# Optimization experiments

Measured on AMD Instinct MI355X. Metric: run time of the kernel, lower is better.

## Reference

```python
import jax, jax.numpy as jnp
import numpy as np

N_PART = 22
N_DIM = 3
H0 = 8
H_SIZE = H0 + 1  # + time condition
HID = 64
N_LAYERS = 4
B = 1024


def _base_edges(n):
    rows, cols = [], []
    for i in range(n):
        for j in range(i + 1, n):
            rows += [i, j]
            cols += [j, i]
    return np.asarray(rows, np.int32), np.asarray(cols, np.int32)


def _batched_edges(n_batch, n_nodes):
    r0, c0 = _base_edges(n_nodes)
    offs = (np.arange(n_batch, dtype=np.int32) * n_nodes)[:, None]
    rows = (r0[None, :] + offs).reshape(-1)
    cols = (c0[None, :] + offs).reshape(-1)
    return jnp.asarray(rows), jnp.asarray(cols)


def setup_inputs() -> dict:
    key = jax.random.key(0)
    ks = jax.random.split(key, 24)
    s = 0.1
    L = N_LAYERS
    d = {
        't': jax.random.uniform(ks[0], (B, 1), jnp.float32),
        'xs': jax.random.normal(ks[1], (B, N_PART * N_DIM), jnp.float32),
        'h_initial': jax.random.normal(ks[2], (N_PART, H0), jnp.float32),
        'emb_w': jax.random.normal(ks[3], (H_SIZE, HID), jnp.float32) * s,
        'emb_b': jnp.zeros((HID,), jnp.float32),
        'emb_out_w': jax.random.normal(ks[4], (HID, H_SIZE), jnp.float32) * s,
        'emb_out_b': jnp.zeros((H_SIZE,), jnp.float32),
        # edge_mlp: in = 2*HID + 1 (radial) + 1 (edge_attr) = 130
        'edge_w1': jax.random.normal(ks[5], (L, 2 * HID + 2, HID), jnp.float32) * s,
        'edge_b1': jnp.zeros((L, HID), jnp.float32),
        'edge_w2': jax.random.normal(ks[6], (L, HID, HID), jnp.float32) * s,
        'edge_b2': jnp.zeros((L, HID), jnp.float32),
        # node_mlp: in = HID (h) + HID (agg) = 128
        'node_w1': jax.random.normal(ks[7], (L, 2 * HID, HID), jnp.float32) * s,
        'node_b1': jnp.zeros((L, HID), jnp.float32),
        'node_w2': jax.random.normal(ks[8], (L, HID, HID), jnp.float32) * s,
        'node_b2': jnp.zeros((L, HID), jnp.float32),
        # coord_mlp: Lin(HID,HID) -> SiLU -> Lin(HID,1, no bias, xavier gain 0.001)
        'coord_w1': jax.random.normal(ks[9], (L, HID, HID), jnp.float32) * s,
        'coord_b1': jnp.zeros((L, HID), jnp.float32),
        'coord_w2': jax.random.normal(ks[10], (L, HID, 1), jnp.float32) * 0.001,
    }
    return d


def _egnn_forward(t, xs, h_initial, emb_w, emb_b, emb_out_w, emb_out_b,
                  edge_w1, edge_b1, edge_w2, edge_b2,
                  node_w1, node_b1, node_w2, node_b2,
                  coord_w1, coord_b1, coord_w2, rows, cols):
    silu = jax.nn.silu
    n_batch = xs.shape[0]
    N = n_batch * N_PART
    x0 = xs[:, :N_PART * N_DIM].reshape(N, N_DIM)

    # node features: atom features tiled over batch + time column
    h = jnp.tile(h_initial[None], (n_batch, 1, 1)).reshape(N, H0)
    t_nodes = jnp.repeat(t.reshape(n_batch, 1), N_PART, axis=0)  # (N,1)
    h = jnp.concatenate([h, t_nodes], axis=-1)  # (N, H_SIZE)

    # static edge attribute: squared distance at input coords
    d0 = x0[rows] - x0[cols]
    edge_attr = jnp.sum(d0 * d0, axis=-1, keepdims=True)  # (E,1)

    h = h @ emb_w + emb_b  # embedding
    x = x0
    for i in range(N_LAYERS):
        diff = x[rows] - x[cols]                       # (E,3)
        radial = jnp.sum(diff * diff, -1, keepdims=True)
        diff = diff / jnp.sqrt(radial + 1e-8)          # norm_diff=True
        ef = jnp.concatenate([h[rows], h[cols], radial, edge_attr], -1)
        m = silu(ef @ edge_w1[i] + edge_b1[i])
        m = silu(m @ edge_w2[i] + edge_b2[i])          # edge messages (E,HID)
        # equivariant coordinate update (tanh=False)
        scal = silu(m @ coord_w1[i] + coord_b1[i]) @ coord_w2[i]  # (E,1)
        x = x + jax.ops.segment_sum(diff * scal, rows, num_segments=N)
        # node update with residual (recurrent=True)
        agg = jax.ops.segment_sum(m, rows, num_segments=N)
        hn = silu(jnp.concatenate([h, agg], -1) @ node_w1[i] + node_b1[i])
        h = h + (hn @ node_w2[i] + node_b2[i])
    _ = h @ emb_out_w + emb_out_b  # embedding_out (h output unused by EGNN_AD2_CV)

    vel = (x - x0).reshape(n_batch, N_PART, N_DIM)
    vel = vel - jnp.mean(vel, axis=1, keepdims=True)   # remove_mean
    return vel.reshape(n_batch, N_PART * N_DIM)


def reference(t, xs, h_initial, emb_w, emb_b, emb_out_w, emb_out_b,
              edge_w1, edge_b1, edge_w2, edge_b2,
              node_w1, node_b1, node_w2, node_b2,
              coord_w1, coord_b1, coord_w2):
    rows, cols = _batched_edges(xs.shape[0], N_PART)
    return _egnn_forward(t, xs, h_initial, emb_w, emb_b, emb_out_w, emb_out_b,
                         edge_w1, edge_b1, edge_w2, edge_b2,
                         node_w1, node_b1, node_w2, node_b2,
                         coord_w1, coord_b1, coord_w2, rows, cols)
```

## Files before the change

kernel.cpp:

```cpp
#include <hip/hip_runtime.h>
#include <hip/hip_bf16.h>

#define NPART 22
#define NDEG  21
#define NEDGE 462
#define HID   64
#define NLAYERS 4
#define NSTRIPB 29
#define MW2S  72

typedef __attribute__((ext_vector_type(8))) short bf16x8;
typedef __attribute__((ext_vector_type(4))) float f32x4;
typedef __attribute__((ext_vector_type(4))) unsigned int u32x4;

__device__ __forceinline__ float silu_f(float v) {
    return __fdividef(v, 1.0f + __expf(-v));
}
__device__ __forceinline__ unsigned short bfu(float v) {
    return __bfloat16_as_ushort(__float2bfloat16(v));
}
__device__ __forceinline__ float bf2f(unsigned h) { return __uint_as_float(h << 16); }

__device__ __forceinline__ void split8(const float* va, bf16x8& hi, bf16x8& lo) {
    #pragma unroll
    for (int i = 0; i < 8; ++i) {
        unsigned short h = bfu(va[i]);
        hi[i] = (short)h;
        lo[i] = (short)bfu(va[i] - bf2f(h));
    }
}

__global__ void prep_wfrag(const float* __restrict__ edge_w2,
                           const float* __restrict__ coord_w1,
                           unsigned* __restrict__ wfrag)
{
    const int m = blockIdx.x;
    const int l = threadIdx.x;
    const int L = m >> 1;
    const float* W = (m & 1) ? (coord_w1 + L*HID*HID) : (edge_w2 + L*HID*HID);
    const int kg = l >> 4, j0 = l & 15;
    u32x4* ws4 = (u32x4*)wfrag;
    #pragma unroll
    for (int nt = 0; nt < 4; ++nt) {
        #pragma unroll
        for (int c = 0; c < 2; ++c) {
            u32x4 p;
            #pragma unroll
            for (int pi = 0; pi < 4; ++pi) {
                int k = c*32 + kg*8 + 2*pi;
                float v0 = W[k*HID + nt*16 + j0];
                float v1 = W[(k+1)*HID + nt*16 + j0];
                p[pi] = (unsigned)bfu(v0) | ((unsigned)bfu(v1) << 16);
            }
            ws4[m*512 + (nt*2 + c)*64 + l] = p;
        }
    }
}

__global__ void prep_nfrag(const float* __restrict__ node_w1,
                           const float* __restrict__ node_w2,
                           const float* __restrict__ edge_w1,
                           unsigned* __restrict__ nfrag)
{
    const int b = blockIdx.x;
    const int L = b >> 2, mat = b & 3;
    const int l = threadIdx.x;
    const int kg = l >> 4, j0 = l & 15;
    u32x4* nf = (u32x4*)nfrag + (size_t)L*80*64;
    const float* W; int nc, base;
    if      (mat == 0) { W = node_w1 + L*2*HID*HID;            nc = 4; base = 0;  }
    else if (mat == 1) { W = node_w2 + L*HID*HID;              nc = 2; base = 16; }
    else if (mat == 2) { W = edge_w1 + (L+1)*130*HID;          nc = 2; base = 24; }
    else               { W = edge_w1 + (L+1)*130*HID + 64*HID; nc = 2; base = 32; }
    for (int nt = 0; nt < 4; ++nt) {
        for (int c = 0; c < nc; ++c) {
            u32x4 ph, pl;
            #pragma unroll
            for (int pi = 0; pi < 4; ++pi) {
                int k = c*32 + kg*8 + 2*pi;
                float v0 = W[k*HID + nt*16 + j0];
                float v1 = W[(k+1)*HID + nt*16 + j0];
                unsigned h0 = bfu(v0), h1 = bfu(v1);
                unsigned l0 = bfu(v0 - bf2f(h0)), l1 = bfu(v1 - bf2f(h1));
                ph[pi] = h0 | (h1 << 16);
                pl[pi] = l0 | (l1 << 16);
            }
            int idx = base + nt*nc + c;
            nf[(size_t)idx*64 + l] = ph;
            nf[(size_t)(40 + idx)*64 + l] = pl;
        }
    }
}

__global__ __launch_bounds__(256, 4)
void k_init(const float* __restrict__ t_in, const float* __restrict__ xs,
            const float* __restrict__ h_init,
            const float* __restrict__ emb_w, const float* __restrict__ emb_b,
            const float* __restrict__ edge_w1, const float* __restrict__ edge_b1,
            float* __restrict__ xw, float* __restrict__ hw,
            float* __restrict__ Hrw, float* __restrict__ Hcw, int NT)
{
    __shared__ __align__(16) float hbuf[4][68];
    const int w = threadIdx.x >> 6, l = threadIdx.x & 63;
    const int n = blockIdx.x*4 + w;
    if (n >= NT) return;
    const int bidx = n / NPART, p = n - bidx*NPART;
    float hv = emb_b[l] + t_in[bidx]*emb_w[8*HID + l];
    #pragma unroll
    for (int k = 0; k < 8; ++k) hv += h_init[p*8 + k]*emb_w[k*HID + l];
    hw[(size_t)n*HID + l] = hv;
    hbuf[w][l] = hv;
    float accr = edge_b1[l], accc = 0.f;
    #pragma unroll 4
    for (int k = 0; k < HID; ++k) {
        float hk = hbuf[w][k];
        accr += hk*edge_w1[k*HID + l];
        accc += hk*edge_w1[(HID + k)*HID + l];
    }
    Hrw[(size_t)n*HID + l] = accr;
    Hcw[(size_t)n*HID + l] = accc;
    if (l < 3) xw[n*3 + l] = xs[n*3 + l];
}

__global__ __launch_bounds__(256, 4)
void k_edgeA(const float* __restrict__ edge_w1v,
             const float* __restrict__ edge_b2L,
             const float* __restrict__ coord_b1L,
             const float* __restrict__ coord_w2L,
             const unsigned* __restrict__ wfrag,
             const float* __restrict__ xs,
             const float* __restrict__ xw,
             const float* __restrict__ Hrw,
             const float* __restrict__ Hcw,
             float* __restrict__ aggpart,
             float* __restrict__ scalg,
             int nstrips, int Lmat)
{
    __shared__ __align__(16) float vecs[5][64];
    __shared__ __align__(16) unsigned short mwall[4][16*MW2S];
    __shared__ __align__(16) float xst[4][2][68];

    const int tid = threadIdx.x, l = tid & 63, w = tid >> 6;
    const int kg = l >> 4, j0 = l & 15;

    for (int i = tid; i < 320; i += 256) {
        int a = i >> 6, o = i & 63; float v;
        if      (a == 0) v = edge_w1v[o];
        else if (a == 1) v = edge_w1v[64 + o];
        else if (a == 2) v = edge_b2L[o];
        else if (a == 3) v = coord_b1L[o];
        else             v = coord_w2L[o];
        vecs[a][o] = v;
    }
    __syncthreads();

    const int sid = blockIdx.x*4 + w;
    if (sid >= nstrips) return;
    const int batch = sid / NSTRIPB, s = sid - batch*NSTRIPB;
    const int e0 = s*16;
    const int ecnt = (NEDGE - e0 < 16) ? (NEDGE - e0) : 16;
    const int n0 = e0 / NDEG;

    {
        const int base = batch*(NPART*3);
        xst[w][0][l] = xw[base + l];
        xst[w][1][l] = xs[base + l];
        if (l < 2) { xst[w][0][64+l] = xw[base+64+l]; xst[w][1][64+l] = xs[base+64+l]; }
    }

    int eg = e0 + j0; if (eg >= NEDGE) eg = NEDGE - 1;
    const int a  = eg / NDEG;
    const int r  = eg - a*NDEG;
    const int bb = r + (r >= a ? 1 : 0);
    float d0 = xst[w][0][a*3+0] - xst[w][0][bb*3+0];
    float d1 = xst[w][0][a*3+1] - xst[w][0][bb*3+1];
    float d2 = xst[w][0][a*3+2] - xst[w][0][bb*3+2];
    float rad = d0*d0 + d1*d1 + d2*d2;
    float g0 = xst[w][1][a*3+0] - xst[w][1][bb*3+0];
    float g1 = xst[w][1][a*3+1] - xst[w][1][bb*3+1];
    float g2 = xst[w][1][a*3+2] - xst[w][1][bb*3+2];
    float eav = g0*g0 + g1*g1 + g2*g2;

    const u32x4* ws4 = (const u32x4*)wfrag;
    const u32x4* wb1 = ws4 + (size_t)(Lmat*2    )*512 + l;
    const u32x4* wb2 = ws4 + (size_t)(Lmat*2 + 1)*512 + l;
    bf16x8 BW1[4][2];
    #pragma unroll
    for (int nt = 0; nt < 4; ++nt) {
        BW1[nt][0] = __builtin_bit_cast(bf16x8, wb1[(nt*2 + 0)*64]);
        BW1[nt][1] = __builtin_bit_cast(bf16x8, wb1[(nt*2 + 1)*64]);
    }

    bf16x8 Ah[2], Al[2];
    {
        const float* hrp = Hrw + (size_t)(batch*NPART + a)*HID;
        const float* hcp = Hcw + (size_t)(batch*NPART + bb)*HID;
        #pragma unroll
        for (int c = 0; c < 2; ++c) {
            const int k0 = c*32 + kg*8;
            float4 ra = *(const float4*)(hrp + k0);
            float4 rb = *(const float4*)(hrp + k0 + 4);
            float4 ca = *(const float4*)(hcp + k0);
            float4 cb = *(const float4*)(hcp + k0 + 4);
            float4 va = *(const float4*)&vecs[0][k0];
            float4 vb = *(const float4*)&vecs[0][k0 + 4];
            float4 ua = *(const float4*)&vecs[1][k0];
            float4 ub = *(const float4*)&vecs[1][k0 + 4];
            float tv[8];
            tv[0] = silu_f(ra.x + ca.x + rad*va.x + eav*ua.x);
            tv[1] = silu_f(ra.y + ca.y + rad*va.y + eav*ua.y);
            tv[2] = silu_f(ra.z + ca.z + rad*va.z + eav*ua.z);
            tv[3] = silu_f(ra.w + ca.w + rad*va.w + eav*ua.w);
            tv[4] = silu_f(rb.x + cb.x + rad*vb.x + eav*ub.x);
            tv[5] = silu_f(rb.y + cb.y + rad*vb.y + eav*ub.y);
            tv[6] = silu_f(rb.z + cb.z + rad*vb.z + eav*ub.z);
            tv[7] = silu_f(rb.w + cb.w + rad*vb.w + eav*ub.w);
            split8(tv, Ah[c], Al[c]);
        }
    }

    f32x4 acc[4];
    #pragma unroll
    for (int nt = 0; nt < 4; ++nt) {
        f32x4 z = {0.f, 0.f, 0.f, 0.f};
        z = __builtin_amdgcn_mfma_f32_16x16x32_bf16(Ah[0], BW1[nt][0], z, 0, 0, 0);
        z = __builtin_amdgcn_mfma_f32_16x16x32_bf16(Al[0], BW1[nt][0], z, 0, 0, 0);
        z = __builtin_amdgcn_mfma_f32_16x16x32_bf16(Ah[1], BW1[nt][1], z, 0, 0, 0);
        z = __builtin_amdgcn_mfma_f32_16x16x32_bf16(Al[1], BW1[nt][1], z, 0, 0, 0);
        acc[nt] = z;
    }

    bf16x8 B2[4][2];
    #pragma unroll
    for (int nt = 0; nt < 4; ++nt) {
        B2[nt][0] = __builtin_bit_cast(bf16x8, wb2[(nt*2 + 0)*64]);
        B2[nt][1] = __builtin_bit_cast(bf16x8, wb2[(nt*2 + 1)*64]);
    }

    int abn[4], emask[4];
    #pragma unroll
    for (int r2 = 0; r2 < 4; ++r2) {
        int e2 = kg*4 + r2;
        int eg2 = e0 + e2; if (eg2 >= NEDGE) eg2 = NEDGE - 1;
        abn[r2] = eg2 / NDEG;
        emask[r2] = (e2 < ecnt);
    }
    unsigned short* mw = mwall[w];
    float p0[4] = {0.f,0.f,0.f,0.f}, p1[4] = {0.f,0.f,0.f,0.f};
    #pragma unroll
    for (int nt = 0; nt < 4; ++nt) {
        int j = nt*16 + j0;
        float bv = vecs[2][j];
        #pragma unroll
        for (int r2 = 0; r2 < 4; ++r2) {
            float mv = silu_f(acc[nt][r2] + bv);
            mw[(kg*4 + r2)*MW2S + j] = bfu(mv);
            float msk = emask[r2] ? mv : 0.f;
            if (abn[r2] == n0)     p0[nt] += msk;
            if (abn[r2] == n0 + 1) p1[nt] += msk;
        }
    }
    #pragma unroll
    for (int nt = 0; nt < 4; ++nt) {
        p0[nt] += __shfl_xor(p0[nt], 16);
        p0[nt] += __shfl_xor(p0[nt], 32);
        p1[nt] += __shfl_xor(p1[nt], 16);
        p1[nt] += __shfl_xor(p1[nt], 32);
    }
    {
        float* apb = aggpart + (size_t)(batch*NSTRIPB + s)*128;
        if (kg == 0) {
            #pragma unroll
            for (int nt = 0; nt < 4; ++nt) apb[nt*16 + j0] = p0[nt];
        } else if (kg == 1) {
            #pragma unroll
            for (int nt = 0; nt < 4; ++nt) apb[64 + nt*16 + j0] = p1[nt];
        }
    }

    bf16x8 A2h[2];
    {
        const unsigned short* arp = mw + j0*MW2S;
        A2h[0] = *(const bf16x8*)(arp + kg*8);
        A2h[1] = *(const bf16x8*)(arp + 32 + kg*8);
    }

    f32x4 acc2[4];
    #pragma unroll
    for (int nt = 0; nt < 4; ++nt) {
        f32x4 z = {0.f, 0.f, 0.f, 0.f};
        z = __builtin_amdgcn_mfma_f32_16x16x32_bf16(A2h[0], B2[nt][0], z, 0, 0, 0);
        z = __builtin_amdgcn_mfma_f32_16x16x32_bf16(A2h[1], B2[nt][1], z, 0, 0, 0);
        acc2[nt] = z;
    }

    float pr[4] = {0.f,0.f,0.f,0.f};
    #pragma unroll
    for (int nt = 0; nt < 4; ++nt) {
        int j = nt*16 + j0;
        float cb = vecs[3][j], cw = vecs[4][j];
        #pragma unroll
        for (int r2 = 0; r2 < 4; ++r2)
            pr[r2] += silu_f(acc2[nt][r2] + cb) * cw;
    }
    #pragma unroll
    for (int off = 8; off > 0; off >>= 1) {
        #pragma unroll
        for (int r2 = 0; r2 < 4; ++r2)
            pr[r2] += __shfl_xor(pr[r2], off);
    }
    if (j0 == 0) {
        #pragma unroll
        for (int r2 = 0; r2 < 4; ++r2) {
            int e2 = kg*4 + r2;
            if (e2 < ecnt) scalg[(size_t)batch*464 + e0 + e2] = pr[r2];
        }
    }
}

__global__ __launch_bounds__(256, 4)
void k_dx(const float* __restrict__ scalg, float* __restrict__ xw, int NB)
{
    __shared__ float xstd[4][68], dxd[4][68];
    const int tid = threadIdx.x, l = tid & 63, w = tid >> 6;
    const int batch = blockIdx.x*4 + w;
    if (batch >= NB) return;
    xstd[w][l] = xw[batch*66 + ((l < 66) ? l : 0)];
    if (l < 2) xstd[w][64 + l] = xw[batch*66 + 64 + l];
    dxd[w][l] = 0.f;
    if (l < 4) dxd[w][64 + l] = 0.f;
    for (int e = l; e < NEDGE; e += 64) {
        int a = e / NDEG, r = e - a*NDEG;
        int bb = r + (r >= a ? 1 : 0);
        float d0 = xstd[w][a*3+0] - xstd[w][bb*3+0];
        float d1 = xstd[w][a*3+1] - xstd[w][bb*3+1];
        float d2 = xstd[w][a*3+2] - xstd[w][bb*3+2];
        float inv = rsqrtf(d0*d0 + d1*d1 + d2*d2 + 1e-8f);
        float sc = scalg[(size_t)batch*464 + e] * inv;
        atomicAdd(&dxd[w][a*3+0], d0*sc);
        atomicAdd(&dxd[w][a*3+1], d1*sc);
        atomicAdd(&dxd[w][a*3+2], d2*sc);
    }
    if (l < 64) xw[batch*66 + ((l < 66) ? l : 0)] = xstd[w][l] + dxd[w][l];
    if (l < 2)  xw[batch*66 + 64 + l] = xstd[w][64 + l] + dxd[w][64 + l];
}

__global__ __launch_bounds__(256, 2)
void k_nodeM(const unsigned* __restrict__ nfragL,
             const float* __restrict__ nb1p, const float* __restrict__ nb2p,
             const float* __restrict__ eb1p,
             const float* __restrict__ aggpart,
             float* __restrict__ hw,
             float* __restrict__ Hrw, float* __restrict__ Hcw,
             int NT, int nstripN)
{
    __shared__ __align__(16) float hT[4][16][68];
    __shared__ __align__(16) float hnT[4][16][68];
    const int tid = threadIdx.x, l = tid & 63, w = tid >> 6;
    const int kg = l >> 4, j0 = l & 15;
    const int sid = blockIdx.x*4 + w;
    if (sid >= nstripN) return;

    {
        int row = l >> 2, cc = (l & 3) << 4;
        int nd = sid*16 + row; if (nd >= NT) nd = NT - 1;
        const float* src = hw + (size_t)nd*HID + cc;
        *(float4*)&hT[w][row][cc]      = *(const float4*)(src);
        *(float4*)&hT[w][row][cc + 4]  = *(const float4*)(src + 4);
        *(float4*)&hT[w][row][cc + 8]  = *(const float4*)(src + 8);
        *(float4*)&hT[w][row][cc + 12] = *(const float4*)(src + 12);
    }

    const int ndl  = sid*16 + j0;
    const int ndc  = (ndl < NT) ? ndl : NT - 1;
    const int bidx = ndc / NPART, p = ndc - bidx*NPART;

    bf16x8 A1h[4], A1l[4];
    #pragma unroll
    for (int c = 0; c < 2; ++c) {
        float tv[8];
        #pragma unroll
        for (int i = 0; i < 8; ++i) tv[i] = hT[w][j0][c*32 + kg*8 + i];
        split8(tv, A1h[c], A1l[c]);
    }
    {
        const int smin = (NDEG*p) >> 4;
        const int smax = (NDEG*p + 20) >> 4;
        #pragma unroll
        for (int c = 2; c < 4; ++c) {
            const int k0a = (c - 2)*32 + kg*8;
            float tv[8] = {0.f,0.f,0.f,0.f,0.f,0.f,0.f,0.f};
            for (int s = smin; s <= smax; ++s) {
                int slot = (p == (s*16)/NDEG) ? 0 : 1;
                const float* ap = aggpart + (size_t)(bidx*NSTRIPB + s)*128 + slot*64 + k0a;
                float4 qa = *(const float4*)ap;
                float4 qb = *(const float4*)(ap + 4);
                tv[0] += qa.x; tv[1] += qa.y; tv[2] += qa.z; tv[3] += qa.w;
                tv[4] += qb.x; tv[5] += qb.y; tv[6] += qb.z; tv[7] += qb.w;
            }
            split8(tv, A1h[c], A1l[c]);
        }
    }

    const u32x4* nf = (const u32x4*)nfragL;
    #define NBF(idx) __builtin_bit_cast(bf16x8, nf[(size_t)(idx)*64 + l])

    f32x4 acc1[4];
    #pragma unroll
    for (int nt = 0; nt < 4; ++nt) {
        f32x4 z = {0.f, 0.f, 0.f, 0.f};
        #pragma unroll
        for (int c = 0; c < 4; ++c) {
            bf16x8 bh = NBF(nt*4 + c), bl = NBF(40 + nt*4 + c);
            z = __builtin_amdgcn_mfma_f32_16x16x32_bf16(A1h[c], bh, z, 0, 0, 0);
            z = __builtin_amdgcn_mfma_f32_16x16x32_bf16(A1l[c], bh, z, 0, 0, 0);
            z = __builtin_amdgcn_mfma_f32_16x16x32_bf16(A1h[c], bl, z, 0, 0, 0);
        }
        acc1[nt] = z;
    }
    #pragma unroll
    for (int nt = 0; nt < 4; ++nt) {
        float bv = nb1p[nt*16 + j0];
        #pragma unroll
        for (int r2 = 0; r2 < 4; ++r2)
            hnT[w][kg*4 + r2][nt*16 + j0] = silu_f(acc1[nt][r2] + bv);
    }

    bf16x8 A2h[2], A2l[2];
    #pragma unroll
    for (int c = 0; c < 2; ++c) {
        float tv[8];
        #pragma unroll
        for (int i = 0; i < 8; ++i) tv[i] = hnT[w][j0][c*32 + kg*8 + i];
        split8(tv, A2h[c], A2l[c]);
    }
    f32x4 acc2[4];
    #pragma unroll
    for (int nt = 0; nt < 4; ++nt) {
        f32x4 z = {0.f, 0.f, 0.f, 0.f};
        #pragma unroll
        for (int c = 0; c < 2; ++c) {
            bf16x8 bh = NBF(16 + nt*2 + c), bl = NBF(56 + nt*2 + c);
            z = __builtin_amdgcn_mfma_f32_16x16x32_bf16(A2h[c], bh, z, 0, 0, 0);
            z = __builtin_amdgcn_mfma_f32_16x16x32_bf16(A2l[c], bh, z, 0, 0, 0);
            z = __builtin_amdgcn_mfma_f32_16x16x32_bf16(A2h[c], bl, z, 0, 0, 0);
        }
        acc2[nt] = z;
    }
    #pragma unroll
    for (int nt = 0; nt < 4; ++nt) {
        float bv = nb2p[nt*16 + j0];
        #pragma unroll
        for (int r2 = 0; r2 < 4; ++r2) {
            int row = kg*4 + r2, col = nt*16 + j0;
            float hv = hT[w][row][col] + acc2[nt][r2] + bv;
            hnT[w][row][col] = hv;
            int nd = sid*16 + row;
            if (nd < NT) hw[(size_t)nd*HID + col] = hv;
        }
    }

    bf16x8 A3h[2], A3l[2];
    #pragma unroll
    for (int c = 0; c < 2; ++c) {
        float tv[8];
        #pragma unroll
        for (int i = 0; i < 8; ++i) tv[i] = hnT[w][j0][c*32 + kg*8 + i];
        split8(tv, A3h[c], A3l[c]);
    }
    f32x4 accR[4], accC[4];
    #pragma unroll
    for (int nt = 0; nt < 4; ++nt) {
        f32x4 zr = {0.f,0.f,0.f,0.f}, zc = {0.f,0.f,0.f,0.f};
        #pragma unroll
        for (int c = 0; c < 2; ++c) {
            bf16x8 brh = NBF(24 + nt*2 + c), brl = NBF(64 + nt*2 + c);
            bf16x8 bch = NBF(32 + nt*2 + c), bcl = NBF(72 + nt*2 + c);
            zr = __builtin_amdgcn_mfma_f32_16x16x32_bf16(A3h[c], brh, zr, 0, 0, 0);
            zr = __builtin_amdgcn_mfma_f32_16x16x32_bf16(A3l[c], brh, zr, 0, 0, 0);
            zr = __builtin_amdgcn_mfma_f32_16x16x32_bf16(A3h[c], brl, zr, 0, 0, 0);
            zc = __builtin_amdgcn_mfma_f32_16x16x32_bf16(A3h[c], bch, zc, 0, 0, 0);
            zc = __builtin_amdgcn_mfma_f32_16x16x32_bf16(A3l[c], bch, zc, 0, 0, 0);
            zc = __builtin_amdgcn_mfma_f32_16x16x32_bf16(A3h[c], bcl, zc, 0, 0, 0);
        }
        accR[nt] = zr; accC[nt] = zc;
    }
    #pragma unroll
    for (int nt = 0; nt < 4; ++nt) {
        float bv = eb1p[nt*16 + j0];
        #pragma unroll
        for (int r2 = 0; r2 < 4; ++r2) {
            int row = kg*4 + r2, col = nt*16 + j0;
            int nd = sid*16 + row;
            if (nd < NT) {
                Hrw[(size_t)nd*HID + col] = accR[nt][r2] + bv;
                Hcw[(size_t)nd*HID + col] = accC[nt][r2];
            }
        }
    }
    #undef NBF
}

__global__ void k_final(const float* __restrict__ xw, const float* __restrict__ xs,
                        const float* __restrict__ scalg, float* __restrict__ out)
{
    __shared__ float xstB[68], dxB[68], vb[68], mv3[3];
    const int b = blockIdx.x, t = threadIdx.x;
    if (t < 66) xstB[t] = xw[b*66 + t];
    if (t < 68) dxB[t] = 0.f;
    __syncthreads();
    for (int e = t; e < NEDGE; e += 256) {
        int a = e / NDEG, r = e - a*NDEG;
        int bb = r + (r >= a ? 1 : 0);
        float d0 = xstB[a*3+0] - xstB[bb*3+0];
        float d1 = xstB[a*3+1] - xstB[bb*3+1];
        float d2 = xstB[a*3+2] - xstB[bb*3+2];
        float inv = rsqrtf(d0*d0 + d1*d1 + d2*d2 + 1e-8f);
        float sc = scalg[(size_t)b*464 + e] * inv;
        atomicAdd(&dxB[a*3+0], d0*sc);
        atomicAdd(&dxB[a*3+1], d1*sc);
        atomicAdd(&dxB[a*3+2], d2*sc);
    }
    __syncthreads();
    if (t < 66) vb[t] = xstB[t] + dxB[t] - xs[b*66 + t];
    __syncthreads();
    if (t < 3) {
        float s = 0.f;
        #pragma unroll
        for (int p = 0; p < NPART; ++p) s += vb[p*3 + t];
        mv3[t] = s / (float)NPART;
    }
    __syncthreads();
    if (t < 66) out[b*66 + t] = vb[t] - mv3[t % 3];
}

extern "C" void kernel_launch(void* const* d_in, const int* in_sizes, int n_in,
                              void* d_out, int out_size, void* d_ws, size_t ws_size,
                              hipStream_t stream) {
    const float* t_in     = (const float*)d_in[0];
    const float* xs       = (const float*)d_in[1];
    const float* h_init   = (const float*)d_in[2];
    const float* emb_w    = (const float*)d_in[3];
    const float* emb_b    = (const float*)d_in[4];
    const float* edge_w1  = (const float*)d_in[7];
    const float* edge_b1  = (const float*)d_in[8];
    const float* edge_w2  = (const float*)d_in[9];
    const float* edge_b2  = (const float*)d_in[10];
    const float* node_w1  = (const float*)d_in[11];
    const float* node_b1  = (const float*)d_in[12];
    const float* node_w2  = (const float*)d_in[13];
    const float* node_b2  = (const float*)d_in[14];
    const float* coord_w1 = (const float*)d_in[15];
    const float* coord_b1 = (const float*)d_in[16];
    const float* coord_w2 = (const float*)d_in[17];
    float* outp = (float*)d_out;

    const int NB = in_sizes[0];
    const int NT = NB * NPART;
    float* xw      = (float*)d_ws;
    float* hw      = xw   + (size_t)NT*3;
    float* Hrw     = hw   + (size_t)NT*HID;
    float* Hcw     = Hrw  + (size_t)NT*HID;
    float* aggpart = Hcw  + (size_t)NT*HID;
    float* scalg   = aggpart + (size_t)NB*NSTRIPB*128;
    unsigned* wfrag = (unsigned*)(scalg + (size_t)NB*464);
    unsigned* nfrag = wfrag + (size_t)8*512*4;

    const int nstrips = NB * NSTRIPB;
    const int gA = (nstrips + 3) / 4;
    const int gI = (NT + 3) / 4;
    const int nstripN = (NT + 15) / 16;
    const int gN = (nstripN + 3) / 4;
    const int gD = (NB + 3) / 4;

    prep_wfrag<<<8, 64, 0, stream>>>(edge_w2, coord_w1, wfrag);
    prep_nfrag<<<12, 64, 0, stream>>>(node_w1, node_w2, edge_w1, nfrag);
    k_init<<<gI, 256, 0, stream>>>(t_in, xs, h_init, emb_w, emb_b,
                                   edge_w1, edge_b1, xw, hw, Hrw, Hcw, NT);
    for (int L = 0; L < NLAYERS; ++L) {
        k_edgeA<<<gA, 256, 0, stream>>>(
            edge_w1 + L*130*HID + 128*HID,
            edge_b2 + L*HID, coord_b1 + L*HID, coord_w2 + L*HID,
            wfrag, xs, xw, Hrw, Hcw, aggpart, scalg, nstrips, L);
        if (L < NLAYERS - 1) {
            k_dx<<<gD, 256, 0, stream>>>(scalg, xw, NB);
            k_nodeM<<<gN, 256, 0, stream>>>(
                nfrag + (size_t)L*80*64*4,
                node_b1 + L*HID, node_b2 + L*HID, edge_b1 + (L+1)*HID,
                aggpart, hw, Hrw, Hcw, NT, nstripN);
        }
    }
    k_final<<<NB, 256, 0, stream>>>(xw, xs, scalg, outp);
}
```

Before: 386.4 us.

## Switch MFMA from split-bf16 to single fp16 and fuse dx/node kernels

```diff
diff --git a/kernel.cpp b/kernel.cpp
--- a/kernel.cpp
+++ b/kernel.cpp
@@ -1,5 +1,5 @@
 #include <hip/hip_runtime.h>
-#include <hip/hip_bf16.h>
+#include <hip/hip_fp16.h>
 
 #define NPART 22
 #define NDEG  21
@@ -9,25 +9,15 @@
 #define NSTRIPB 29
 #define MW2S  72
 
-typedef __attribute__((ext_vector_type(8))) short bf16x8;
+typedef _Float16 f16x8 __attribute__((ext_vector_type(8)));
 typedef __attribute__((ext_vector_type(4))) float f32x4;
 typedef __attribute__((ext_vector_type(4))) unsigned int u32x4;
 
 __device__ __forceinline__ float silu_f(float v) {
     return __fdividef(v, 1.0f + __expf(-v));
 }
-__device__ __forceinline__ unsigned short bfu(float v) {
-    return __bfloat16_as_ushort(__float2bfloat16(v));
-}
-__device__ __forceinline__ float bf2f(unsigned h) { return __uint_as_float(h << 16); }
-
-__device__ __forceinline__ void split8(const float* va, bf16x8& hi, bf16x8& lo) {
-    #pragma unroll
-    for (int i = 0; i < 8; ++i) {
-        unsigned short h = bfu(va[i]);
-        hi[i] = (short)h;
-        lo[i] = (short)bfu(va[i] - bf2f(h));
-    }
+__device__ __forceinline__ unsigned short hfu(float v) {
+    return __half_as_ushort(__float2half(v));
 }
 
 __global__ void prep_wfrag(const float* __restrict__ edge_w2,
@@ -50,7 +40,7 @@
                 int k = c*32 + kg*8 + 2*pi;
                 float v0 = W[k*HID + nt*16 + j0];
                 float v1 = W[(k+1)*HID + nt*16 + j0];
-                p[pi] = (unsigned)bfu(v0) | ((unsigned)bfu(v1) << 16);
+                p[pi] = (unsigned)hfu(v0) | ((unsigned)hfu(v1) << 16);
             }
             ws4[m*512 + (nt*2 + c)*64 + l] = p;
         }
@@ -66,7 +56,7 @@
     const int L = b >> 2, mat = b & 3;
     const int l = threadIdx.x;
     const int kg = l >> 4, j0 = l & 15;
-    u32x4* nf = (u32x4*)nfrag + (size_t)L*80*64;
+    u32x4* nf = (u32x4*)nfrag + (size_t)L*40*64;
     const float* W; int nc, base;
     if      (mat == 0) { W = node_w1 + L*2*HID*HID;            nc = 4; base = 0;  }
     else if (mat == 1) { W = node_w2 + L*HID*HID;              nc = 2; base = 16; }
@@ -74,20 +64,15 @@
     else               { W = edge_w1 + (L+1)*130*HID + 64*HID; nc = 2; base = 32; }
     for (int nt = 0; nt < 4; ++nt) {
         for (int c = 0; c < nc; ++c) {
-            u32x4 ph, pl;
+            u32x4 p;
             #pragma unroll
             for (int pi = 0; pi < 4; ++pi) {
                 int k = c*32 + kg*8 + 2*pi;
                 float v0 = W[k*HID + nt*16 + j0];
                 float v1 = W[(k+1)*HID + nt*16 + j0];
-                unsigned h0 = bfu(v0), h1 = bfu(v1);
-                unsigned l0 = bfu(v0 - bf2f(h0)), l1 = bfu(v1 - bf2f(h1));
-                ph[pi] = h0 | (h1 << 16);
-                pl[pi] = l0 | (l1 << 16);
+                p[pi] = (unsigned)hfu(v0) | ((unsigned)hfu(v1) << 16);
             }
-            int idx = base + nt*nc + c;
-            nf[(size_t)idx*64 + l] = ph;
-            nf[(size_t)(40 + idx)*64 + l] = pl;
+            nf[(size_t)(base + nt*nc + c)*64 + l] = p;
         }
     }
 }
@@ -136,23 +121,11 @@
              float* __restrict__ scalg,
              int nstrips, int Lmat)
 {
-    __shared__ __align__(16) float vecs[5][64];
     __shared__ __align__(16) unsigned short mwall[4][16*MW2S];
     __shared__ __align__(16) float xst[4][2][68];
 
     const int tid = threadIdx.x, l = tid & 63, w = tid >> 6;
     const int kg = l >> 4, j0 = l & 15;
-
-    for (int i = tid; i < 320; i += 256) {
-        int a = i >> 6, o = i & 63; float v;
-        if      (a == 0) v = edge_w1v[o];
-        else if (a == 1) v = edge_w1v[64 + o];
-        else if (a == 2) v = edge_b2L[o];
-        else if (a == 3) v = coord_b1L[o];
-        else             v = coord_w2L[o];
-        vecs[a][o] = v;
-    }
-    __syncthreads();
 
     const int sid = blockIdx.x*4 + w;
     if (sid >= nstrips) return;
@@ -184,14 +157,14 @@
     const u32x4* ws4 = (const u32x4*)wfrag;
     const u32x4* wb1 = ws4 + (size_t)(Lmat*2    )*512 + l;
     const u32x4* wb2 = ws4 + (size_t)(Lmat*2 + 1)*512 + l;
-    bf16x8 BW1[4][2];
-    #pragma unroll
-    for (int nt = 0; nt < 4; ++nt) {
-        BW1[nt][0] = __builtin_bit_cast(bf16x8, wb1[(nt*2 + 0)*64]);
-        BW1[nt][1] = __builtin_bit_cast(bf16x8, wb1[(nt*2 + 1)*64]);
-    }
-
-    bf16x8 Ah[2], Al[2];
+    f16x8 BW1[4][2];
+    #pragma unroll
+    for (int nt = 0; nt < 4; ++nt) {
+        BW1[nt][0] = __builtin_bit_cast(f16x8, wb1[(nt*2 + 0)*64]);
+        BW1[nt][1] = __builtin_bit_cast(f16x8, wb1[(nt*2 + 1)*64]);
+    }
+
+    f16x8 A1[2];
     {
         const float* hrp = Hrw + (size_t)(batch*NPART + a)*HID;
         const float* hcp = Hcw + (size_t)(batch*NPART + bb)*HID;
@@ -202,20 +175,20 @@
             float4 rb = *(const float4*)(hrp + k0 + 4);
             float4 ca = *(const float4*)(hcp + k0);
             float4 cb = *(const float4*)(hcp + k0 + 4);
-            float4 va = *(const float4*)&vecs[0][k0];
-            float4 vb = *(const float4*)&vecs[0][k0 + 4];
-            float4 ua = *(const float4*)&vecs[1][k0];
-            float4 ub = *(const float4*)&vecs[1][k0 + 4];
-            float tv[8];
-            tv[0] = silu_f(ra.x + ca.x + rad*va.x + eav*ua.x);
-            tv[1] = silu_f(ra.y + ca.y + rad*va.y + eav*ua.y);
-            tv[2] = silu_f(ra.z + ca.z + rad*va.z + eav*ua.z);
-            tv[3] = silu_f(ra.w + ca.w + rad*va.w + eav*ua.w);
-            tv[4] = silu_f(rb.x + cb.x + rad*vb.x + eav*ub.x);
-            tv[5] = silu_f(rb.y + cb.y + rad*vb.y + eav*ub.y);
-            tv[6] = silu_f(rb.z + cb.z + rad*vb.z + eav*ub.z);
-            tv[7] = silu_f(rb.w + cb.w + rad*vb.w + eav*ub.w);
-            split8(tv, Ah[c], Al[c]);
+            float4 va = *(const float4*)(edge_w1v + k0);
+            float4 vb = *(const float4*)(edge_w1v + k0 + 4);
+            float4 ua = *(const float4*)(edge_w1v + 64 + k0);
+            float4 ub = *(const float4*)(edge_w1v + 64 + k0 + 4);
+            f16x8 A;
+            A[0] = (_Float16)silu_f(ra.x + ca.x + rad*va.x + eav*ua.x);
+            A[1] = (_Float16)silu_f(ra.y + ca.y + rad*va.y + eav*ua.y);
+            A[2] = (_Float16)silu_f(ra.z + ca.z + rad*va.z + eav*ua.z);
+            A[3] = (_Float16)silu_f(ra.w + ca.w + rad*va.w + eav*ua.w);
+            A[4] = (_Float16)silu_f(rb.x + cb.x + rad*vb.x + eav*ub.x);
+            A[5] = (_Float16)silu_f(rb.y + cb.y + rad*vb.y + eav*ub.y);
+            A[6] = (_Float16)silu_f(rb.z + cb.z + rad*vb.z + eav*ub.z);
+            A[7] = (_Float16)silu_f(rb.w + cb.w + rad*vb.w + eav*ub.w);
+            A1[c] = A;
         }
     }
 
@@ -223,74 +196,71 @@
     #pragma unroll
     for (int nt = 0; nt < 4; ++nt) {
         f32x4 z = {0.f, 0.f, 0.f, 0.f};
-        z = __builtin_amdgcn_mfma_f32_16x16x32_bf16(Ah[0], BW1[nt][0], z, 0, 0, 0);
-        z = __builtin_amdgcn_mfma_f32_16x16x32_bf16(Al[0], BW1[nt][0], z, 0, 0, 0);
-        z = __builtin_amdgcn_mfma_f32_16x16x32_bf16(Ah[1], BW1[nt][1], z, 0, 0, 0);
-        z = __builtin_amdgcn_mfma_f32_16x16x32_bf16(Al[1], BW1[nt][1], z, 0, 0, 0);
+        z = __builtin_amdgcn_mfma_f32_16x16x32_f16(A1[0], BW1[nt][0], z, 0, 0, 0);
+        z = __builtin_amdgcn_mfma_f32_16x16x32_f16(A1[1], BW1[nt][1], z, 0, 0, 0);
         acc[nt] = z;
     }
 
-    bf16x8 B2[4][2];
-    #pragma unroll
-    for (int nt = 0; nt < 4; ++nt) {
-        B2[nt][0] = __builtin_bit_cast(bf16x8, wb2[(nt*2 + 0)*64]);
-        B2[nt][1] = __builtin_bit_cast(bf16x8, wb2[(nt*2 + 1)*64]);
-    }
-
-    int abn[4], emask[4];
+    f16x8 B2[4][2];
+    #pragma unroll
+    for (int nt = 0; nt < 4; ++nt) {
+        B2[nt][0] = __builtin_bit_cast(f16x8, wb2[(nt*2 + 0)*64]);
+        B2[nt][1] = __builtin_bit_cast(f16x8, wb2[(nt*2 + 1)*64]);
+    }
+
+    int sel[4], emask[4];
     #pragma unroll
     for (int r2 = 0; r2 < 4; ++r2) {
         int e2 = kg*4 + r2;
         int eg2 = e0 + e2; if (eg2 >= NEDGE) eg2 = NEDGE - 1;
-        abn[r2] = eg2 / NDEG;
+        sel[r2] = (eg2 / NDEG == n0);
         emask[r2] = (e2 < ecnt);
     }
     unsigned short* mw = mwall[w];
-    float p0[4] = {0.f,0.f,0.f,0.f}, p1[4] = {0.f,0.f,0.f,0.f};
+    float pS[4] = {0.f,0.f,0.f,0.f}, pT[4] = {0.f,0.f,0.f,0.f};
     #pragma unroll
     for (int nt = 0; nt < 4; ++nt) {
         int j = nt*16 + j0;
-        float bv = vecs[2][j];
+        float bv = edge_b2L[j];
         #pragma unroll
         for (int r2 = 0; r2 < 4; ++r2) {
-            float mv = silu_f(acc[nt][r2] + bv);
-            mw[(kg*4 + r2)*MW2S + j] = bfu(mv);
-            float msk = emask[r2] ? mv : 0.f;
-            if (abn[r2] == n0)     p0[nt] += msk;
-            if (abn[r2] == n0 + 1) p1[nt] += msk;
-        }
-    }
-    #pragma unroll
-    for (int nt = 0; nt < 4; ++nt) {
-        p0[nt] += __shfl_xor(p0[nt], 16);
-        p0[nt] += __shfl_xor(p0[nt], 32);
-        p1[nt] += __shfl_xor(p1[nt], 16);
-        p1[nt] += __shfl_xor(p1[nt], 32);
+            float mv = emask[r2] ? silu_f(acc[nt][r2] + bv) : 0.f;
+            mw[(kg*4 + r2)*MW2S + j] = hfu(mv);
+            pT[nt] += mv;
+            pS[nt] += sel[r2] ? mv : 0.f;
+        }
+    }
+    #pragma unroll
+    for (int nt = 0; nt < 4; ++nt) {
+        pS[nt] += __shfl_xor(pS[nt], 16);
+        pS[nt] += __shfl_xor(pS[nt], 32);
+        pT[nt] += __shfl_xor(pT[nt], 16);
+        pT[nt] += __shfl_xor(pT[nt], 32);
     }
     {
         float* apb = aggpart + (size_t)(batch*NSTRIPB + s)*128;
         if (kg == 0) {
             #pragma unroll
-            for (int nt = 0; nt < 4; ++nt) apb[nt*16 + j0] = p0[nt];
+            for (int nt = 0; nt < 4; ++nt) apb[nt*16 + j0] = pS[nt];
         } else if (kg == 1) {
             #pragma unroll
-            for (int nt = 0; nt < 4; ++nt) apb[64 + nt*16 + j0] = p1[nt];
-        }
-    }
-
-    bf16x8 A2h[2];
+            for (int nt = 0; nt < 4; ++nt) apb[64 + nt*16 + j0] = pT[nt] - pS[nt];
+        }
+    }
+
+    f16x8 A2[2];
     {
         const unsigned short* arp = mw + j0*MW2S;
-        A2h[0] = *(const bf16x8*)(arp + kg*8);
-        A2h[1] = *(const bf16x8*)(arp + 32 + kg*8);
+        A2[0] = *(const f16x8*)(arp + kg*8);
+        A2[1] = *(const f16x8*)(arp + 32 + kg*8);
     }
 
     f32x4 acc2[4];
     #pragma unroll
     for (int nt = 0; nt < 4; ++nt) {
         f32x4 z = {0.f, 0.f, 0.f, 0.f};
-        z = __builtin_amdgcn_mfma_f32_16x16x32_bf16(A2h[0], B2[nt][0], z, 0, 0, 0);
-        z = __builtin_amdgcn_mfma_f32_16x16x32_bf16(A2h[1], B2[nt][1], z, 0, 0, 0);
+        z = __builtin_amdgcn_mfma_f32_16x16x32_f16(A2[0], B2[nt][0], z, 0, 0, 0);
+        z = __builtin_amdgcn_mfma_f32_16x16x32_f16(A2[1], B2[nt][1], z, 0, 0, 0);
         acc2[nt] = z;
     }
 
@@ -298,7 +268,7 @@
     #pragma unroll
     for (int nt = 0; nt < 4; ++nt) {
         int j = nt*16 + j0;
-        float cb = vecs[3][j], cw = vecs[4][j];
+        float cb = coord_b1L[j], cw = coord_w2L[j];
         #pragma unroll
         for (int r2 = 0; r2 < 4; ++r2)
             pr[r2] += silu_f(acc2[nt][r2] + cb) * cw;
@@ -318,47 +288,47 @@
     }
 }
 
-__global__ __launch_bounds__(256, 4)
-void k_dx(const float* __restrict__ scalg, float* __restrict__ xw, int NB)
-{
-    __shared__ float xstd[4][68], dxd[4][68];
-    const int tid = threadIdx.x, l = tid & 63, w = tid >> 6;
-    const int batch = blockIdx.x*4 + w;
-    if (batch >= NB) return;
-    xstd[w][l] = xw[batch*66 + ((l < 66) ? l : 0)];
-    if (l < 2) xstd[w][64 + l] = xw[batch*66 + 64 + l];
-    dxd[w][l] = 0.f;
-    if (l < 4) dxd[w][64 + l] = 0.f;
-    for (int e = l; e < NEDGE; e += 64) {
-        int a = e / NDEG, r = e - a*NDEG;
-        int bb = r + (r >= a ? 1 : 0);
-        float d0 = xstd[w][a*3+0] - xstd[w][bb*3+0];
-        float d1 = xstd[w][a*3+1] - xstd[w][bb*3+1];
-        float d2 = xstd[w][a*3+2] - xstd[w][bb*3+2];
-        float inv = rsqrtf(d0*d0 + d1*d1 + d2*d2 + 1e-8f);
-        float sc = scalg[(size_t)batch*464 + e] * inv;
-        atomicAdd(&dxd[w][a*3+0], d0*sc);
-        atomicAdd(&dxd[w][a*3+1], d1*sc);
-        atomicAdd(&dxd[w][a*3+2], d2*sc);
-    }
-    if (l < 64) xw[batch*66 + ((l < 66) ? l : 0)] = xstd[w][l] + dxd[w][l];
-    if (l < 2)  xw[batch*66 + 64 + l] = xstd[w][64 + l] + dxd[w][64 + l];
-}
-
 __global__ __launch_bounds__(256, 2)
-void k_nodeM(const unsigned* __restrict__ nfragL,
-             const float* __restrict__ nb1p, const float* __restrict__ nb2p,
-             const float* __restrict__ eb1p,
-             const float* __restrict__ aggpart,
-             float* __restrict__ hw,
-             float* __restrict__ Hrw, float* __restrict__ Hcw,
-             int NT, int nstripN)
+void k_dxnode(const float* __restrict__ scalg, float* __restrict__ xw, int NB, int gD,
+              const unsigned* __restrict__ nfragL,
+              const float* __restrict__ nb1p, const float* __restrict__ nb2p,
+              const float* __restrict__ eb1p,
+              const float* __restrict__ aggpart,
+              float* __restrict__ hw,
+              float* __restrict__ Hrw, float* __restrict__ Hcw,
+              int NT, int nstripN)
 {
     __shared__ __align__(16) float hT[4][16][68];
     __shared__ __align__(16) float hnT[4][16][68];
+    __shared__ float xstd[4][68], dxd[4][68];
     const int tid = threadIdx.x, l = tid & 63, w = tid >> 6;
     const int kg = l >> 4, j0 = l & 15;
-    const int sid = blockIdx.x*4 + w;
+
+    if (blockIdx.x < (unsigned)gD) {
+        const int batch = blockIdx.x*4 + w;
+        if (batch >= NB) return;
+        xstd[w][l] = xw[batch*66 + ((l < 66) ? l : 0)];
+        if (l < 2) xstd[w][64 + l] = xw[batch*66 + 64 + l];
+        dxd[w][l] = 0.f;
+        if (l < 4) dxd[w][64 + l] = 0.f;
+        for (int e = l; e < NEDGE; e += 64) {
+            int a = e / NDEG, r = e - a*NDEG;
+            int bb = r + (r >= a ? 1 : 0);
+            float d0 = xstd[w][a*3+0] - xstd[w][bb*3+0];
+            float d1 = xstd[w][a*3+1] - xstd[w][bb*3+1];
+            float d2 = xstd[w][a*3+2] - xstd[w][bb*3+2];
+            float inv = rsqrtf(d0*d0 + d1*d1 + d2*d2 + 1e-8f);
+            float sc = scalg[(size_t)batch*464 + e] * inv;
+            atomicAdd(&dxd[w][a*3+0], d0*sc);
+            atomicAdd(&dxd[w][a*3+1], d1*sc);
+            atomicAdd(&dxd[w][a*3+2], d2*sc);
+        }
+        xw[batch*66 + ((l < 66) ? l : 0)] = xstd[w][l] + dxd[w][l];
+        if (l < 2) xw[batch*66 + 64 + l] = xstd[w][64 + l] + dxd[w][64 + l];
+        return;
+    }
+
+    const int sid = (blockIdx.x - gD)*4 + w;
     if (sid >= nstripN) return;
 
     {
@@ -375,13 +345,13 @@
     const int ndc  = (ndl < NT) ? ndl : NT - 1;
     const int bidx = ndc / NPART, p = ndc - bidx*NPART;
 
-    bf16x8 A1h[4], A1l[4];
+    f16x8 A1[4];
     #pragma unroll
     for (int c = 0; c < 2; ++c) {
-        float tv[8];
-        #pragma unroll
-        for (int i = 0; i < 8; ++i) tv[i] = hT[w][j0][c*32 + kg*8 + i];
-        split8(tv, A1h[c], A1l[c]);
+        f16x8 A;
+        #pragma unroll
+        for (int i = 0; i < 8; ++i) A[i] = (_Float16)hT[w][j0][c*32 + kg*8 + i];
+        A1[c] = A;
     }
     {
         const int smin = (NDEG*p) >> 4;
@@ -398,24 +368,23 @@
                 tv[0] += qa.x; tv[1] += qa.y; tv[2] += qa.z; tv[3] += qa.w;
                 tv[4] += qb.x; tv[5] += qb.y; tv[6] += qb.z; tv[7] += qb.w;
             }
-            split8(tv, A1h[c], A1l[c]);
+            f16x8 A;
+            #pragma unroll
+            for (int i = 0; i < 8; ++i) A[i] = (_Float16)tv[i];
+            A1[c] = A;
         }
     }
 
     const u32x4* nf = (const u32x4*)nfragL;
-    #define NBF(idx) __builtin_bit_cast(bf16x8, nf[(size_t)(idx)*64 + l])
+    #define NBF(idx) __builtin_bit_cast(f16x8, nf[(size_t)(idx)*64 + l])
 
     f32x4 acc1[4];
     #pragma unroll
     for (int nt = 0; nt < 4; ++nt) {
         f32x4 z = {0.f, 0.f, 0.f, 0.f};
         #pragma unroll
-        for (int c = 0; c < 4; ++c) {
-            bf16x8 bh = NBF(nt*4 + c), bl = NBF(40 + nt*4 + c);
-            z = __builtin_amdgcn_mfma_f32_16x16x32_bf16(A1h[c], bh, z, 0, 0, 0);
-            z = __builtin_amdgcn_mfma_f32_16x16x32_bf16(A1l[c], bh, z, 0, 0, 0);
-            z = __builtin_amdgcn_mfma_f32_16x16x32_bf16(A1h[c], bl, z, 0, 0, 0);
-        }
+        for (int c = 0; c < 4; ++c)
+            z = __builtin_amdgcn_mfma_f32_16x16x32_f16(A1[c], NBF(nt*4 + c), z, 0, 0, 0);
         acc1[nt] = z;
     }
     #pragma unroll
@@ -426,25 +395,21 @@
             hnT[w][kg*4 + r2][nt*16 + j0] = silu_f(acc1[nt][r2] + bv);
     }
 
-    bf16x8 A2h[2], A2l[2];
+    f16x8 A2[2];
     #pragma unroll
     for (int c = 0; c < 2; ++c) {
-        float tv[8];
-        #pragma unroll
-        for (int i = 0; i < 8; ++i) tv[i] = hnT[w][j0][c*32 + kg*8 + i];
-        split8(tv, A2h[c], A2l[c]);
+        f16x8 A;
+        #pragma unroll
+        for (int i = 0; i < 8; ++i) A[i] = (_Float16)hnT[w][j0][c*32 + kg*8 + i];
+        A2[c] = A;
     }
     f32x4 acc2[4];
     #pragma unroll
     for (int nt = 0; nt < 4; ++nt) {
         f32x4 z = {0.f, 0.f, 0.f, 0.f};
         #pragma unroll
-        for (int c = 0; c < 2; ++c) {
-            bf16x8 bh = NBF(16 + nt*2 + c), bl = NBF(56 + nt*2 + c);
-            z = __builtin_amdgcn_mfma_f32_16x16x32_bf16(A2h[c], bh, z, 0, 0, 0);
-            z = __builtin_amdgcn_mfma_f32_16x16x32_bf16(A2l[c], bh, z, 0, 0, 0);
-            z = __builtin_amdgcn_mfma_f32_16x16x32_bf16(A2h[c], bl, z, 0, 0, 0);
-        }
+        for (int c = 0; c < 2; ++c)
+            z = __builtin_amdgcn_mfma_f32_16x16x32_f16(A2[c], NBF(16 + nt*2 + c), z, 0, 0, 0);
         acc2[nt] = z;
     }
     #pragma unroll
@@ -460,13 +425,13 @@
         }
     }
 
-    bf16x8 A3h[2], A3l[2];
+    f16x8 A3[2];
     #pragma unroll
     for (int c = 0; c < 2; ++c) {
-        float tv[8];
-        #pragma unroll
-        for (int i = 0; i < 8; ++i) tv[i] = hnT[w][j0][c*32 + kg*8 + i];
-        split8(tv, A3h[c], A3l[c]);
+        f16x8 A;
+        #pragma unroll
+        for (int i = 0; i < 8; ++i) A[i] = (_Float16)hnT[w][j0][c*32 + kg*8 + i];
+        A3[c] = A;
     }
     f32x4 accR[4], accC[4];
     #pragma unroll
@@ -474,14 +439,8 @@
         f32x4 zr = {0.f,0.f,0.f,0.f}, zc = {0.f,0.f,0.f,0.f};
         #pragma unroll
         for (int c = 0; c < 2; ++c) {
-            bf16x8 brh = NBF(24 + nt*2 + c), brl = NBF(64 + nt*2 + c);
-            bf16x8 bch = NBF(32 + nt*2 + c), bcl = NBF(72 + nt*2 + c);
-            zr = __builtin_amdgcn_mfma_f32_16x16x32_bf16(A3h[c], brh, zr, 0, 0, 0);
-            zr = __builtin_amdgcn_mfma_f32_16x16x32_bf16(A3l[c], brh, zr, 0, 0, 0);
-            zr = __builtin_amdgcn_mfma_f32_16x16x32_bf16(A3h[c], brl, zr, 0, 0, 0);
-            zc = __builtin_amdgcn_mfma_f32_16x16x32_bf16(A3h[c], bch, zc, 0, 0, 0);
-            zc = __builtin_amdgcn_mfma_f32_16x16x32_bf16(A3l[c], bch, zc, 0, 0, 0);
-            zc = __builtin_amdgcn_mfma_f32_16x16x32_bf16(A3h[c], bcl, zc, 0, 0, 0);
+            zr = __builtin_amdgcn_mfma_f32_16x16x32_f16(A3[c], NBF(24 + nt*2 + c), zr, 0, 0, 0);
+            zc = __builtin_amdgcn_mfma_f32_16x16x32_f16(A3[c], NBF(32 + nt*2 + c), zc, 0, 0, 0);
         }
         accR[nt] = zr; accC[nt] = zc;
     }
@@ -583,9 +542,9 @@
             edge_b2 + L*HID, coord_b1 + L*HID, coord_w2 + L*HID,
             wfrag, xs, xw, Hrw, Hcw, aggpart, scalg, nstrips, L);
         if (L < NLAYERS - 1) {
-            k_dx<<<gD, 256, 0, stream>>>(scalg, xw, NB);
-            k_nodeM<<<gN, 256, 0, stream>>>(
-                nfrag + (size_t)L*80*64*4,
+            k_dxnode<<<gD + gN, 256, 0, stream>>>(
+                scalg, xw, NB, gD,
+                nfrag + (size_t)L*40*64*4,
                 node_b1 + L*HID, node_b2 + L*HID, edge_b1 + (L+1)*HID,
                 aggpart, hw, Hrw, Hcw, NT, nstripN);
         }
```

Measured after the change: 354.8 us. 1.09x faster.
